# Optimization experiments

Measured on AMD Instinct MI355X. Metric: run time of the kernel, lower is better.

The kernel has to match this reference:

```python
import jax, jax.numpy as jnp
import numpy as np

SEQ_LEN, BATCH, INPUT_SIZE, HIDDEN_SIZE = 2048, 512, 64, 128


def setup_inputs() -> dict:
    key = jax.random.key(0)
    kx, k1, kb1, k2, kb2 = jax.random.split(key, 5)
    s1 = 1.0 / np.sqrt(INPUT_SIZE)
    s2 = 1.0 / np.sqrt(HIDDEN_SIZE)
    return {
        "x": jax.random.normal(kx, (SEQ_LEN, BATCH, INPUT_SIZE), dtype=jnp.float32),
        "W1": jax.random.uniform(k1, (HIDDEN_SIZE, INPUT_SIZE), jnp.float32, -s1, s1),
        "b1": jax.random.uniform(kb1, (HIDDEN_SIZE,), jnp.float32, -s1, s1),
        "W2": jax.random.uniform(k2, (HIDDEN_SIZE, HIDDEN_SIZE), jnp.float32, -s2, s2),
        "b2": jax.random.uniform(kb2, (HIDDEN_SIZE,), jnp.float32, -s2, s2),
    }


def reference(x, W1, b1, W2, b2):
    # Elman RNN: h_t = tanh(fc2(h_{t-1}) + fc1(x_t)), h_0 = 0
    # x: (S, B, I); W1: (H, I); W2: (H, H)
    B = x.shape[1]
    H = W2.shape[0]
    h0 = jnp.zeros((B, H), dtype=x.dtype)

    def step(h, x_t):
        h_new = jnp.tanh(x_t @ W1.T + b1 + h @ W2.T + b2)
        return h_new, h_new

    h_last, h_seq = jax.lax.scan(step, h0, x)
    return h_seq, h_last[None]  # (S,B,H), (1,B,H)
```

## Files before the change

kernel.cpp:

```cpp
#include <hip/hip_runtime.h>
#include <math.h>


#define S_LEN 2048
#define B_SZ  512
#define I_SZ  64
#define H_SZ  128
#define BT    16
#define NTILE 32
#define BLK   512
#define SPB   8
#define SBH   (B_SZ * H_SZ)

typedef short bf16x8 __attribute__((ext_vector_type(8)));
typedef float f32x4  __attribute__((ext_vector_type(4)));

#define MFMA(A, B, C) __builtin_amdgcn_mfma_f32_16x16x32_bf16((A), (B), (C), 0, 0, 0)

#define LDS_BARRIER()                                        \
    asm volatile("s_waitcnt lgkmcnt(0)" ::: "memory");       \
    __builtin_amdgcn_s_barrier();                            \
    asm volatile("" ::: "memory")

__device__ __forceinline__ unsigned fbits(float v) {
    union { float f; unsigned u; } x; x.f = v; return x.u;
}
__device__ __forceinline__ float fval(unsigned u) {
    union { float f; unsigned u; } x; x.u = u; return x.f;
}
__device__ __forceinline__ unsigned short bf_trunc(float v) {
    return (unsigned short)(fbits(v) >> 16);
}
__device__ __forceinline__ void split8t(float4 a, float4 b, bf16x8* hi, bf16x8* lo) {
    float v[8] = {a.x, a.y, a.z, a.w, b.x, b.y, b.z, b.w};
    #pragma unroll
    for (int j = 0; j < 8; ++j) {
        unsigned short h = bf_trunc(v[j]);
        (*hi)[j] = (short)h;
        (*lo)[j] = (short)bf_trunc(v[j] - fval(((unsigned)h) << 16));
    }
}

__global__ __launch_bounds__(BLK) void rnn_prepass(
    const float* __restrict__ x,
    const float* __restrict__ W1,
    const float* __restrict__ b1,
    const float* __restrict__ b2,
    float* __restrict__ z)
{
    const int tid  = threadIdx.x;
    const int lane = tid & 63;
    const int w    = tid >> 6;
    const int l15  = lane & 15;
    const int l4   = lane >> 4;
    const int unit = (w << 4) + l15;
    const int bid  = blockIdx.x;
    const int tile = bid & (NTILE - 1);
    const int s0   = (bid >> 5) * SPB;
    const int b0   = tile << 4;

    bf16x8 w1h[2], w1l[2];
    #pragma unroll
    for (int c = 0; c < 2; ++c) {
        const float* wr = W1 + unit * I_SZ + 32 * c + l4 * 8;
        split8t(*(const float4*)wr, *(const float4*)(wr + 4), &w1h[c], &w1l[c]);
    }
    const float zb = b1[unit] + b2[unit];

    for (int i = 0; i < SPB; ++i) {
        const int s = s0 + i;
        const float* xr = x + ((size_t)s * B_SZ + b0 + l15) * I_SZ + l4 * 8;
        bf16x8 xh[2], xl[2];
        #pragma unroll
        for (int c = 0; c < 2; ++c)
            split8t(*(const float4*)(xr + 32 * c), *(const float4*)(xr + 32 * c + 4),
                    &xh[c], &xl[c]);

        f32x4 acc  = {zb, zb, zb, zb};
        f32x4 acc2 = {0.f, 0.f, 0.f, 0.f};
        acc  = MFMA(xh[0], w1h[0], acc);   acc  = MFMA(xh[1], w1h[1], acc);
        acc2 = MFMA(xl[0], w1h[0], acc2);  acc2 = MFMA(xl[1], w1h[1], acc2);
        acc2 = MFMA(xh[0], w1l[0], acc2);  acc2 = MFMA(xh[1], w1l[1], acc2);
        acc += acc2;

        *(f32x4*)(z + ((size_t)(s * NTILE + tile) * 8 + w) * 256 + lane * 4) = acc;
    }
}

__global__ __launch_bounds__(BLK, 2) void rnn_recur(
    const float* __restrict__ W2,
    const float* zr,
    float* out)
{
    const int tid  = threadIdx.x;
    const int lane = tid & 63;
    const int w    = tid >> 6;
    const int l15  = lane & 15;
    const int l4   = lane >> 4;
    const int unit = (w << 4) + l15;
    const int tile = blockIdx.x;
    const int b0   = tile << 4;

    __shared__ short hp_hi[2][BT * H_SZ];
    __shared__ short hp_lo[2][BT * H_SZ];

    bf16x8 w2h[4], w2l[4];
    #pragma unroll
    for (int c = 0; c < 4; ++c) {
        const float* wr = W2 + unit * H_SZ + 32 * c + l4 * 8;
        split8t(*(const float4*)wr, *(const float4*)(wr + 4), &w2h[c], &w2l[c]);
    }

    int hro[4], woh[4];
    #pragma unroll
    for (int c = 0; c < 4; ++c)
        hro[c] = l15 * 256 + ((64 * c + 16 * l4) ^ ((l15 & 7) << 4));
    #pragma unroll
    for (int r = 0; r < 4; ++r) {
        int row = (l4 << 2) + r;
        woh[r] = row * 256 + ((unit * 2) ^ ((row & 7) << 4));
    }

    const float* zp = zr + (size_t)tile * 2048 + (size_t)w * 256 + lane * 4;
    float* po = out + (size_t)(b0 + (l4 << 2)) * H_SZ + unit;

    f32x4 zA = *(const f32x4*)(zp);
    f32x4 zB = *(const f32x4*)(zp + SBH);

    bf16x8 ah[4], al[4];
    #pragma unroll
    for (int c = 0; c < 4; ++c) { ah[c] = (bf16x8){0,0,0,0,0,0,0,0}; al[c] = ah[c]; }
    float tl[4] = {0.f, 0.f, 0.f, 0.f};

#define BODY(S, P, ZQ)                                                        \
{                                                                             \
    f32x4 acc  = ZQ;                                                          \
    f32x4 acc2 = {0.f, 0.f, 0.f, 0.f};                                        \
    f32x4 acc3 = {0.f, 0.f, 0.f, 0.f};                                        \
          \
    { int sp = (S) + 2; if (sp > S_LEN - 1) sp = S_LEN - 1;                   \
      ZQ = *(const f32x4*)(zp + (size_t)sp * SBH); }                          \
    acc  = MFMA(ah[0], w2h[0], acc);   acc2 = MFMA(al[0], w2h[0], acc2);      \
    acc3 = MFMA(ah[0], w2l[0], acc3);                                         \
    acc  = MFMA(ah[1], w2h[1], acc);   acc2 = MFMA(al[1], w2h[1], acc2);      \
    acc3 = MFMA(ah[1], w2l[1], acc3);                                         \
    acc  = MFMA(ah[2], w2h[2], acc);   acc2 = MFMA(al[2], w2h[2], acc2);      \
    acc3 = MFMA(ah[2], w2l[2], acc3);                                         \
    acc  = MFMA(ah[3], w2h[3], acc);   acc2 = MFMA(al[3], w2h[3], acc2);      \
    acc3 = MFMA(ah[3], w2l[3], acc3);                                         \
    acc = (acc + acc2) + acc3;                                                \
    _Pragma("unroll")                                                         \
    for (int r = 0; r < 4; ++r) {                                             \
        float a = acc[r];                                                     \
        float t = 1.0f - 2.0f * __builtin_amdgcn_rcpf(1.0f + __expf(2.0f*a)); \
        tl[r] = t;                                                            \
        po[(size_t)(S) * SBH + (size_t)r * H_SZ] = t;                         \
        unsigned short hi = bf_trunc(t);                                      \
        *(short*)((char*)hp_hi[P] + woh[r]) = (short)hi;                      \
        *(short*)((char*)hp_lo[P] + woh[r]) =                                 \
            (short)bf_trunc(t - fval(((unsigned)hi) << 16));                  \
    }                                                                         \
    LDS_BARRIER();                                                            \
    _Pragma("unroll")                                                         \
    for (int c = 0; c < 4; ++c) {                                             \
        ah[c] = *(const bf16x8*)((const char*)hp_hi[P] + hro[c]);             \
        al[c] = *(const bf16x8*)((const char*)hp_lo[P] + hro[c]);             \
    }                                                                         \
}

    for (int s2 = 0; s2 < S_LEN; s2 += 2) {
        BODY(s2,     0, zA);
        BODY(s2 + 1, 1, zB);
    }
#undef BODY

    #pragma unroll
    for (int r = 0; r < 4; ++r)
        po[(size_t)S_LEN * SBH + (size_t)r * H_SZ] = tl[r];
}

extern "C" void kernel_launch(void* const* d_in, const int* in_sizes, int n_in,
                              void* d_out, int out_size, void* d_ws, size_t ws_size,
                              hipStream_t stream) {
    const float* x  = (const float*)d_in[0];
    const float* W1 = (const float*)d_in[1];
    const float* b1 = (const float*)d_in[2];
    const float* W2 = (const float*)d_in[3];
    const float* b2 = (const float*)d_in[4];
    float* out = (float*)d_out;

    rnn_prepass<<<dim3((S_LEN / SPB) * NTILE), dim3(BLK), 0, stream>>>(x, W1, b1, b2, out);
    rnn_recur<<<dim3(NTILE), dim3(BLK), 0, stream>>>(W2, out, out);
}
```

Before: 1.477 ms.

## Split recurrence into 64 blocks of 8 batch rows with 4 waves each

The recurrent kernel now uses 64 blocks of 256 threads, each owning 8 batch rows instead of 16, so twice as many CUs carry the serial chain. Each wave computes two 16-unit output tiles, and half the MFMA rows, which come from the padded 16-row tile, are masked out. The prepass writes z in a matching layout. Output stores are moved after the LDS barrier to take them off the critical path. This adds wasted MFMA work on the padded rows and doubles the weight registers per wave.

```diff
diff --git a/kernel.cpp b/kernel.cpp
--- a/kernel.cpp
+++ b/kernel.cpp
@@ -6,9 +6,9 @@
 #define B_SZ  512
 #define I_SZ  64
 #define H_SZ  128
-#define BT    16
 #define NTILE 32
-#define BLK   512
+#define BLK1  512
+#define BLK2  256
 #define SPB   8
 #define SBH   (B_SZ * H_SZ)
 
@@ -41,7 +41,7 @@
     }
 }
 
-__global__ __launch_bounds__(BLK) void rnn_prepass(
+__global__ __launch_bounds__(BLK1) void rnn_prepass(
     const float* __restrict__ x,
     const float* __restrict__ W1,
     const float* __restrict__ b1,
@@ -67,6 +67,9 @@
     }
     const float zb = b1[unit] + b2[unit];
 
+    float* zo = z + (size_t)(s0 * NTILE + tile) * 2048 +
+                (size_t)(l4 >> 1) * 1024 + w * 128 + (l4 & 1) * 64 + l15 * 4;
+
     for (int i = 0; i < SPB; ++i) {
         const int s = s0 + i;
         const float* xr = x + ((size_t)s * B_SZ + b0 + l15) * I_SZ + l4 * 8;
@@ -83,82 +86,100 @@
         acc2 = MFMA(xh[0], w1l[0], acc2);  acc2 = MFMA(xh[1], w1l[1], acc2);
         acc += acc2;
 
-        *(f32x4*)(z + ((size_t)(s * NTILE + tile) * 8 + w) * 256 + lane * 4) = acc;
-    }
-}
-
-__global__ __launch_bounds__(BLK, 2) void rnn_recur(
+        *(f32x4*)(zo + (size_t)i * (NTILE * 2048)) = acc;
+    }
+}
+
+__global__ __launch_bounds__(BLK2, 1) void rnn_recur(
     const float* __restrict__ W2,
     const float* zr,
     float* out)
 {
     const int tid  = threadIdx.x;
     const int lane = tid & 63;
-    const int w    = tid >> 6;
+    const int W    = tid >> 6;
     const int l15  = lane & 15;
     const int l4   = lane >> 4;
-    const int unit = (w << 4) + l15;
-    const int tile = blockIdx.x;
-    const int b0   = tile << 4;
-
-    __shared__ short hp_hi[2][BT * H_SZ];
-    __shared__ short hp_lo[2][BT * H_SZ];
-
-    bf16x8 w2h[4], w2l[4];
-    #pragma unroll
-    for (int c = 0; c < 4; ++c) {
-        const float* wr = W2 + unit * H_SZ + 32 * c + l4 * 8;
-        split8t(*(const float4*)wr, *(const float4*)(wr + 4), &w2h[c], &w2l[c]);
-    }
-
-    int hro[4], woh[4];
+    const int t8   = blockIdx.x;
+    const int b0   = t8 << 3;
+
+    __shared__ short hp_hi[2][8 * H_SZ];
+    __shared__ short hp_lo[2][8 * H_SZ];
+
+    bf16x8 w2h[2][4], w2l[2][4];
+    #pragma unroll
+    for (int st = 0; st < 2; ++st) {
+        const int n = (W << 5) + (st << 4) + l15;
+        #pragma unroll
+        for (int c = 0; c < 4; ++c) {
+            const float* wr = W2 + n * H_SZ + 32 * c + l4 * 8;
+            split8t(*(const float4*)wr, *(const float4*)(wr + 4),
+                    &w2h[st][c], &w2l[st][c]);
+        }
+    }
+
+    const int row8 = l15 & 7;
+    int hro[4];
     #pragma unroll
     for (int c = 0; c < 4; ++c)
-        hro[c] = l15 * 256 + ((64 * c + 16 * l4) ^ ((l15 & 7) << 4));
-    #pragma unroll
-    for (int r = 0; r < 4; ++r) {
-        int row = (l4 << 2) + r;
-        woh[r] = row * 256 + ((unit * 2) ^ ((row & 7) << 4));
-    }
-
-    const float* zp = zr + (size_t)tile * 2048 + (size_t)w * 256 + lane * 4;
-    float* po = out + (size_t)(b0 + (l4 << 2)) * H_SZ + unit;
-
-    f32x4 zA = *(const f32x4*)(zp);
-    f32x4 zB = *(const f32x4*)(zp + SBH);
+        hro[c] = row8 * 256 + ((64 * c + 16 * l4) ^ (row8 << 4));
+    const int rwb = (l4 & 1) << 2;
+    int woh[2][4];
+    #pragma unroll
+    for (int st = 0; st < 2; ++st)
+        #pragma unroll
+        for (int r = 0; r < 4; ++r) {
+            int row = rwb + r;
+            woh[st][r] = row * 256 +
+                ((((W << 5) + (st << 4) + l15) * 2) ^ (row << 4));
+        }
+    const bool wmask = (l4 < 2);
+
+    const float* zp0 = zr + (size_t)b0 * H_SZ +
+                       (size_t)(2 * W) * 128 + (l4 & 1) * 64 + l15 * 4;
+    const float* zp1 = zp0 + 128;
+
+    float* po0 = out + (size_t)(b0 + rwb) * H_SZ + (W << 5) + l15;
+    float* po1 = po0 + 16;
+
+    f32x4 zA0 = *(const f32x4*)(zp0);
+    f32x4 zA1 = *(const f32x4*)(zp1);
+    f32x4 zB0 = *(const f32x4*)(zp0 + SBH);
+    f32x4 zB1 = *(const f32x4*)(zp1 + SBH);
 
     bf16x8 ah[4], al[4];
     #pragma unroll
     for (int c = 0; c < 4; ++c) { ah[c] = (bf16x8){0,0,0,0,0,0,0,0}; al[c] = ah[c]; }
-    float tl[4] = {0.f, 0.f, 0.f, 0.f};
-
-#define BODY(S, P, ZQ)                                                        \
+    float tl0[4], tl1[4];
+
+#define BODY(S, P, Z0, Z1)                                                    \
 {                                                                             \
-    f32x4 acc  = ZQ;                                                          \
-    f32x4 acc2 = {0.f, 0.f, 0.f, 0.f};                                        \
-    f32x4 acc3 = {0.f, 0.f, 0.f, 0.f};                                        \
-          \
+    f32x4 a0 = Z0, a1 = Z1;                                                   \
+    f32x4 b0v = {0.f,0.f,0.f,0.f}, b1v = b0v, c0v = b0v, c1v = b0v;           \
     { int sp = (S) + 2; if (sp > S_LEN - 1) sp = S_LEN - 1;                   \
-      ZQ = *(const f32x4*)(zp + (size_t)sp * SBH); }                          \
-    acc  = MFMA(ah[0], w2h[0], acc);   acc2 = MFMA(al[0], w2h[0], acc2);      \
-    acc3 = MFMA(ah[0], w2l[0], acc3);                                         \
-    acc  = MFMA(ah[1], w2h[1], acc);   acc2 = MFMA(al[1], w2h[1], acc2);      \
-    acc3 = MFMA(ah[1], w2l[1], acc3);                                         \
-    acc  = MFMA(ah[2], w2h[2], acc);   acc2 = MFMA(al[2], w2h[2], acc2);      \
-    acc3 = MFMA(ah[2], w2l[2], acc3);                                         \
-    acc  = MFMA(ah[3], w2h[3], acc);   acc2 = MFMA(al[3], w2h[3], acc2);      \
-    acc3 = MFMA(ah[3], w2l[3], acc3);                                         \
-    acc = (acc + acc2) + acc3;                                                \
+      Z0 = *(const f32x4*)(zp0 + (size_t)sp * SBH);                           \
+      Z1 = *(const f32x4*)(zp1 + (size_t)sp * SBH); }                         \
+    _Pragma("unroll")                                                         \
+    for (int c = 0; c < 4; ++c) {                                             \
+        a0  = MFMA(ah[c], w2h[0][c], a0);   a1  = MFMA(ah[c], w2h[1][c], a1); \
+        b0v = MFMA(al[c], w2h[0][c], b0v);  b1v = MFMA(al[c], w2h[1][c], b1v);\
+        c0v = MFMA(ah[c], w2l[0][c], c0v);  c1v = MFMA(ah[c], w2l[1][c], c1v);\
+    }                                                                         \
+    a0 = (a0 + b0v) + c0v;  a1 = (a1 + b1v) + c1v;                            \
     _Pragma("unroll")                                                         \
     for (int r = 0; r < 4; ++r) {                                             \
-        float a = acc[r];                                                     \
-        float t = 1.0f - 2.0f * __builtin_amdgcn_rcpf(1.0f + __expf(2.0f*a)); \
-        tl[r] = t;                                                            \
-        po[(size_t)(S) * SBH + (size_t)r * H_SZ] = t;                         \
-        unsigned short hi = bf_trunc(t);                                      \
-        *(short*)((char*)hp_hi[P] + woh[r]) = (short)hi;                      \
-        *(short*)((char*)hp_lo[P] + woh[r]) =                                 \
-            (short)bf_trunc(t - fval(((unsigned)hi) << 16));                  \
+        float u0 = 1.0f - 2.0f * __builtin_amdgcn_rcpf(1.0f + __expf(2.0f*a0[r])); \
+        float u1 = 1.0f - 2.0f * __builtin_amdgcn_rcpf(1.0f + __expf(2.0f*a1[r])); \
+        tl0[r] = u0;  tl1[r] = u1;                                            \
+        if (wmask) {                                                          \
+            unsigned short h0 = bf_trunc(u0), h1 = bf_trunc(u1);              \
+            *(short*)((char*)hp_hi[P] + woh[0][r]) = (short)h0;               \
+            *(short*)((char*)hp_lo[P] + woh[0][r]) =                          \
+                (short)bf_trunc(u0 - fval(((unsigned)h0) << 16));             \
+            *(short*)((char*)hp_hi[P] + woh[1][r]) = (short)h1;               \
+            *(short*)((char*)hp_lo[P] + woh[1][r]) =                          \
+                (short)bf_trunc(u1 - fval(((unsigned)h1) << 16));             \
+        }                                                                     \
     }                                                                         \
     LDS_BARRIER();                                                            \
     _Pragma("unroll")                                                         \
@@ -166,17 +187,29 @@
         ah[c] = *(const bf16x8*)((const char*)hp_hi[P] + hro[c]);             \
         al[c] = *(const bf16x8*)((const char*)hp_lo[P] + hro[c]);             \
     }                                                                         \
+     \
+    if (wmask) {                                                              \
+        _Pragma("unroll")                                                     \
+        for (int r = 0; r < 4; ++r) {                                         \
+            po0[(size_t)(S) * SBH + (size_t)r * H_SZ] = tl0[r];               \
+            po1[(size_t)(S) * SBH + (size_t)r * H_SZ] = tl1[r];               \
+        }                                                                     \
+    }                                                                         \
 }
 
     for (int s2 = 0; s2 < S_LEN; s2 += 2) {
-        BODY(s2,     0, zA);
-        BODY(s2 + 1, 1, zB);
+        BODY(s2,     0, zA0, zA1);
+        BODY(s2 + 1, 1, zB0, zB1);
     }
 #undef BODY
 
-    #pragma unroll
-    for (int r = 0; r < 4; ++r)
-        po[(size_t)S_LEN * SBH + (size_t)r * H_SZ] = tl[r];
+    if (wmask) {
+        #pragma unroll
+        for (int r = 0; r < 4; ++r) {
+            po0[(size_t)S_LEN * SBH + (size_t)r * H_SZ] = tl0[r];
+            po1[(size_t)S_LEN * SBH + (size_t)r * H_SZ] = tl1[r];
+        }
+    }
 }
 
 extern "C" void kernel_launch(void* const* d_in, const int* in_sizes, int n_in,
@@ -189,6 +222,6 @@
     const float* b2 = (const float*)d_in[4];
     float* out = (float*)d_out;
 
-    rnn_prepass<<<dim3((S_LEN / SPB) * NTILE), dim3(BLK), 0, stream>>>(x, W1, b1, b2, out);
-    rnn_recur<<<dim3(NTILE), dim3(BLK), 0, stream>>>(W2, out, out);
-}
+    rnn_prepass<<<dim3((S_LEN / SPB) * NTILE), dim3(BLK1), 0, stream>>>(x, W1, b1, b2, out);
+    rnn_recur<<<dim3(2 * NTILE), dim3(BLK2), 0, stream>>>(W2, out, out);
+}
```

New measurement: 1.855 ms. +25.6%, slower.
